# Kernel tuning notes

Hardware: AMD Instinct MI355X
Metric: run time of the kernel (lower is better)

## Reference

```python
import jax, jax.numpy as jnp
import numpy as np

T = 4096
HIDDEN = 2048
N_HEADS = 16
N_KV_HEADS = 4
HEAD_DIM = 128
WINDOW = 1024  # per_layer_sliding_window = WINDOW + 1 -> q attends keys with q_pos - k_pos <= WINDOW
ROPE_THETA = 100000.0
QKV_OUT = (N_HEADS + 2 * N_KV_HEADS) * HEAD_DIM  # 3072


def setup_inputs() -> dict:
    key = jax.random.key(0)
    k1, k2, k3, k4 = jax.random.split(key, 4)
    return {
        "hidden_states": jax.random.normal(k1, (T, HIDDEN), dtype=jnp.float32),
        "positions": jnp.arange(T, dtype=jnp.int32),
        "w_qkv": jax.random.normal(k2, (HIDDEN, QKV_OUT), dtype=jnp.float32) * 0.02,
        "b_qkv": jax.random.normal(k3, (QKV_OUT,), dtype=jnp.float32) * 0.02,
        "w_o": jax.random.normal(k4, (N_HEADS * HEAD_DIM, HIDDEN), dtype=jnp.float32) * 0.02,
    }


def _apply_rope(x, positions):
    # x: [T, n_heads, HEAD_DIM], neox-style rotary over full head dim
    half = HEAD_DIM // 2
    inv_freq = 1.0 / (ROPE_THETA ** (jnp.arange(half, dtype=jnp.float32) / half))
    freqs = positions.astype(jnp.float32)[:, None] * inv_freq[None, :]  # [T, half]
    cos = jnp.cos(freqs)[:, None, :]  # [T, 1, half]
    sin = jnp.sin(freqs)[:, None, :]
    x1, x2 = x[..., :half], x[..., half:]
    return jnp.concatenate([x1 * cos - x2 * sin, x2 * cos + x1 * sin], axis=-1)


def reference(hidden_states, positions, w_qkv, b_qkv, w_o):
    # QKV projection (bias=True)
    qkv = hidden_states @ w_qkv + b_qkv  # [T, QKV_OUT]
    q_size = N_HEADS * HEAD_DIM
    kv_size = N_KV_HEADS * HEAD_DIM
    q = qkv[:, :q_size].reshape(T, N_HEADS, HEAD_DIM)
    k = qkv[:, q_size:q_size + kv_size].reshape(T, N_KV_HEADS, HEAD_DIM)
    v = qkv[:, q_size + kv_size:].reshape(T, N_KV_HEADS, HEAD_DIM)

    # RoPE on q and k
    q = _apply_rope(q, positions)
    k = _apply_rope(k, positions)

    # GQA: expand kv heads to match query heads
    group = N_HEADS // N_KV_HEADS
    k = jnp.repeat(k, group, axis=1)  # [T, N_HEADS, HEAD_DIM]
    v = jnp.repeat(v, group, axis=1)

    scale = HEAD_DIM ** -0.5
    scores = jnp.einsum('qhd,khd->hqk', q, k) * scale  # [H, T, T]

    # causal + sliding-window mask: j <= i and i - j <= WINDOW
    i = jnp.arange(T)[:, None]
    j = jnp.arange(T)[None, :]
    mask = (j <= i) & (i - j <= WINDOW)  # [T, T]
    scores = jnp.where(mask[None, :, :], scores, jnp.finfo(scores.dtype).min)

    probs = jax.nn.softmax(scores, axis=-1)
    attn = jnp.einsum('hqk,khd->qhd', probs, v)  # [T, H, HEAD_DIM]
    attn = attn.reshape(T, N_HEADS * HEAD_DIM)

    # output projection (bias=False)
    return attn @ w_o
```

## Files before the change

### kernel.cpp

```cpp
#include <hip/hip_runtime.h>
#include <cstdint>

#define T_TOK 4096
#define HID 2048
#define NH 16
#define NKV 4
#define HD 128
#define WIN 1024
#define QKVO 3072

typedef float f32x4 __attribute__((ext_vector_type(4)));
typedef float f32x16 __attribute__((ext_vector_type(16)));
typedef __bf16 bf16x8 __attribute__((ext_vector_type(8)));
typedef __bf16 bf16x4 __attribute__((ext_vector_type(4)));
typedef unsigned int u32x4 __attribute__((ext_vector_type(4)));

__device__ __forceinline__ void gload16(const void* g, void* lds) {
  auto gp = reinterpret_cast<__attribute__((address_space(1))) void*>(
      reinterpret_cast<uintptr_t>(g));
  auto lp = reinterpret_cast<__attribute__((address_space(3))) void*>(
      reinterpret_cast<uintptr_t>(lds));
  __builtin_amdgcn_global_load_lds(gp, lp, 16, 0, 0);
}

__device__ __forceinline__ f32x4 mfma16(bf16x8 a, bf16x8 b, f32x4 c) {
  return __builtin_amdgcn_mfma_f32_16x16x32_bf16(a, b, c, 0, 0, 0);
}
__device__ __forceinline__ f32x16 mfma32(bf16x8 a, bf16x8 b, f32x16 c) {
  return __builtin_amdgcn_mfma_f32_32x32x16_bf16(a, b, c, 0, 0, 0);
}
__device__ __forceinline__ unsigned cvtpk(float lo, float hi) {
  unsigned r;
  asm("v_cvt_pk_bf16_f32 %0, %1, %2" : "=v"(r) : "v"(lo), "v"(hi));
  return r;
}
__device__ __forceinline__ void pl32swap(unsigned& a, unsigned& b) {
  asm volatile("v_permlane32_swap_b32 %0, %1" : "+v"(a), "+v"(b));
}

__global__ __launch_bounds__(256) void k_f32_to_bf16(const float* __restrict__ x,
                                                     __bf16* __restrict__ y) {
  const size_t e = (size_t)blockIdx.x * 256 + threadIdx.x;
  const float4* xv = (const float4*)x;
  float4 a = xv[e * 2], b = xv[e * 2 + 1];
  bf16x8 o;
  o[0] = (__bf16)a.x; o[1] = (__bf16)a.y; o[2] = (__bf16)a.z; o[3] = (__bf16)a.w;
  o[4] = (__bf16)b.x; o[5] = (__bf16)b.y; o[6] = (__bf16)b.z; o[7] = (__bf16)b.w;
  *(bf16x8*)(y + e * 8) = o;
}

__global__ __launch_bounds__(256) void k_transpose(const float* __restrict__ W,
                                                   __bf16* __restrict__ Wt,
                                                   int R, int C) {
  __shared__ __bf16 tb[32][33];
  const int nbx = C >> 5;
  const int c0 = (blockIdx.x % nbx) << 5;
  const int r0 = (blockIdx.x / nbx) << 5;
  const int tx = threadIdx.x & 31, ty = threadIdx.x >> 5;
#pragma unroll
  for (int i = 0; i < 32; i += 8)
    tb[ty + i][tx] = (__bf16)W[(size_t)(r0 + ty + i) * C + c0 + tx];
  __syncthreads();
#pragma unroll
  for (int i = 0; i < 32; i += 8)
    Wt[(size_t)(c0 + ty + i) * R + r0 + tx] = tb[tx][ty + i];
}

__global__ void k_rope_tab(const int* __restrict__ pos, float* __restrict__ cosT,
                           float* __restrict__ sinT) {
  const int t = blockIdx.x;
  const int d = threadIdx.x;
  const float inv = exp2f(-(float)d * (16.609640474436812f / 64.0f));
  const float fr = (float)pos[t] * inv;
  cosT[t * 64 + d] = cosf(fr);
  sinT[t * 64 + d] = sinf(fr);
}

template <bool BIAS, typename OutT>
__global__ __launch_bounds__(256, 2) void k_gemm(const __bf16* __restrict__ A,
                                                 const __bf16* __restrict__ Bt,
                                                 const float* __restrict__ bias,
                                                 OutT* __restrict__ C,
                                                 int M, int N, int K) {
  __shared__ __align__(16) __bf16 As[2][128 * 64];
  __shared__ __align__(16) __bf16 Bs[2][128 * 64];
  const int tid = threadIdx.x;
  const int lane = tid & 63;
  const int w = tid >> 6;
  const int wr = w >> 1, wc = w & 1;
  const int c = lane & 15, g = lane >> 4;
  const int csw = (c & 7) << 4;

  const int nstc = N >> 9;
  const int bid = blockIdx.x;
  const int xcd = bid & 7;
  const int j = bid >> 3;
  const int spx = (int)(gridDim.x >> 7);
  const int s = xcd * spx + (j >> 4);
  const int q = j & 15;
  const int by = (s / nstc) * 4 + (q >> 2);
  const int bx = (s % nstc) * 4 + (q & 3);
  const int m0 = by << 7, n0 = bx << 7;

  const int o0 = w * 4096 + lane * 16;
  const int srow = 32 * w + (lane >> 3);
  const int schunk = (lane & 7) ^ ((lane >> 3) & 7);
  const __bf16* gA0 = A + (size_t)(m0 + srow) * K + schunk * 8;
  const __bf16* gB0 = Bt + (size_t)(n0 + srow) * K + schunk * 8;

  f32x4 acc[4][4] = {};

  {
    char* la = (char*)&As[0][0];
    char* lb = (char*)&Bs[0][0];
#pragma unroll
    for (int qq = 0; qq < 4; qq++) {
      gload16(gA0 + (size_t)qq * 8 * K, la + o0 + qq * 1024);
      gload16(gB0 + (size_t)qq * 8 * K, lb + o0 + qq * 1024);
    }
  }
  __syncthreads();

  int cur = 0;
  for (int kt = 0; kt < K; kt += 64) {
    if (kt + 64 < K) {
      char* la = (char*)&As[0][0] + (cur ^ 1) * 16384;
      char* lb = (char*)&Bs[0][0] + (cur ^ 1) * 16384;
#pragma unroll
      for (int qq = 0; qq < 4; qq++) {
        gload16(gA0 + kt + 64 + (size_t)qq * 8 * K, la + o0 + qq * 1024);
        gload16(gB0 + kt + 64 + (size_t)qq * 8 * K, lb + o0 + qq * 1024);
      }
    }
    const char* as = (const char*)&As[0][0] + cur * 16384;
    const char* bs = (const char*)&Bs[0][0] + cur * 16384;
#pragma unroll
    for (int ds = 0; ds < 2; ds++) {
      bf16x8 af[4], bfr[4];
#pragma unroll
      for (int mi = 0; mi < 4; mi++)
        af[mi] = *(const bf16x8*)(as + (wr * 64 + mi * 16 + c) * 128 +
                                  ((ds * 64 + g * 16) ^ csw));
#pragma unroll
      for (int ni = 0; ni < 4; ni++)
        bfr[ni] = *(const bf16x8*)(bs + (wc * 64 + ni * 16 + c) * 128 +
                                   ((ds * 64 + g * 16) ^ csw));
#pragma unroll
      for (int mi = 0; mi < 4; mi++)
#pragma unroll
        for (int ni = 0; ni < 4; ni++)
          acc[mi][ni] = mfma16(af[mi], bfr[ni], acc[mi][ni]);
    }
    __syncthreads();
    cur ^= 1;
  }

#pragma unroll
  for (int ni = 0; ni < 4; ni++) {
    const int col = n0 + wc * 64 + ni * 16 + c;
    const float bv = BIAS ? bias[col] : 0.0f;
#pragma unroll
    for (int mi = 0; mi < 4; mi++)
#pragma unroll
      for (int r = 0; r < 4; r++) {
        const int row = m0 + wr * 64 + mi * 16 + 4 * g + r;
        C[(size_t)row * N + col] = (OutT)(acc[mi][ni][r] + bv);
      }
  }
}

__global__ __launch_bounds__(256) void k_rope_pack(
    const __bf16* __restrict__ qkv, const float* __restrict__ cosT,
    const float* __restrict__ sinT, __bf16* __restrict__ Qp,
    __bf16* __restrict__ Kp, __bf16* __restrict__ Vt) {
  const int t0 = blockIdx.x * 64;
  const int hh = blockIdx.y;
  const int tid = threadIdx.x;
  const int col0 = hh * HD;
  __shared__ __bf16 lt[64][136];
  if (hh < NH + NKV) {
    const bool isq = hh < NH;
    const float s = isq ? (0.08838834764831845f * 1.4426950408889634f) : 1.0f;
    __bf16* base = isq ? (Qp + (size_t)hh * T_TOK * HD)
                       : (Kp + (size_t)(hh - NH) * T_TOK * HD);
#pragma unroll
    for (int jj = 0; jj < 2; jj++) {
      const int e = jj * 256 + tid;
      const int tl = e >> 3, ch = e & 7;
      const int tt = t0 + tl;
      const bf16x8 x1 = *(const bf16x8*)(qkv + (size_t)tt * QKVO + col0 + ch * 8);
      const bf16x8 x2 = *(const bf16x8*)(qkv + (size_t)tt * QKVO + col0 + 64 + ch * 8);
      const float4 c0 = *(const float4*)(cosT + tt * 64 + ch * 8);
      const float4 c1 = *(const float4*)(cosT + tt * 64 + ch * 8 + 4);
      const float4 s0 = *(const float4*)(sinT + tt * 64 + ch * 8);
      const float4 s1 = *(const float4*)(sinT + tt * 64 + ch * 8 + 4);
      const float cs[8] = {c0.x, c0.y, c0.z, c0.w, c1.x, c1.y, c1.z, c1.w};
      const float sn[8] = {s0.x, s0.y, s0.z, s0.w, s1.x, s1.y, s1.z, s1.w};
      bf16x8 o1, o2;
#pragma unroll
      for (int i = 0; i < 8; i++) {
        const float a = (float)x1[i], b = (float)x2[i];
        o1[i] = (__bf16)((a * cs[i] - b * sn[i]) * s);
        o2[i] = (__bf16)((b * cs[i] + a * sn[i]) * s);
      }
      const int d2s = isq ? ch * 8 : ((ch * 8) ^ ((tt & 7) << 3));
      __bf16* dst = base + (size_t)tt * HD;
      *(bf16x8*)(dst + d2s) = o1;
      *(bf16x8*)(dst + 64 + d2s) = o2;
    }
  } else {
    const int kv = hh - (NH + NKV);
#pragma unroll
    for (int jj = 0; jj < 4; jj++) {
      const int e = jj * 256 + tid;
      const int tl = e >> 4, dc = e & 15;
      *(bf16x8*)&lt[tl][dc * 8] =
          *(const bf16x8*)(qkv + (size_t)(t0 + tl) * QKVO + col0 + dc * 8);
    }
    __syncthreads();
#pragma unroll
    for (int jj = 0; jj < 32; jj++) {
      const int e = jj * 256 + tid;
      const int d = e >> 6, tl = e & 63;
      Vt[((size_t)kv * HD + d) * T_TOK + t0 + (tl ^ ((d & 7) << 3))] = lt[tl][d];
    }
  }
}

__global__ __launch_bounds__(256, 2) void k_attn(const __bf16* __restrict__ Qp,
                                                 const __bf16* __restrict__ Kp,
                                                 const __bf16* __restrict__ Vt,
                                                 __bf16* __restrict__ attnO) {
  __shared__ __align__(16) __bf16 Ks[2][64 * 128];
  __shared__ __align__(16) __bf16 Vs[2][128 * 64];

  const int tid = threadIdx.x;
  const int lane = tid & 63;
  const int w = tid >> 6;
  const int l31 = lane & 31;
  const int hi = lane >> 5;
  const int swz = (lane & 7) << 4;
  const int h = blockIdx.y;
  const int kvh = h >> 2;
  const int qb = (int)(gridDim.x - 1) - (int)blockIdx.x;
  const int q0 = qb * 128;
  const int iw = q0 + 32 * w;
  const int irow = iw + l31;

  bf16x8 qf[8];
  {
    const __bf16* qbase = Qp + ((size_t)h * T_TOK + irow) * HD;
#pragma unroll
    for (int ds = 0; ds < 8; ds++)
      qf[ds] = *(const bf16x8*)(qbase + ds * 16 + hi * 8);
  }

  f32x16 ot[4] = {};
  float mrun = 0.0f, lrun = 0.0f;

  const int jstart = (q0 >= WIN) ? (q0 - WIN) : 0;
  const int niter = (q0 + 128 - jstart) >> 6;

  const char* Kg = (const char*)Kp + (size_t)kvh * T_TOK * HD * 2;
  const char* Vg = (const char*)Vt + (size_t)kvh * HD * T_TOK * 2;
  const char* kg0 = Kg + (size_t)(jstart + 16 * w + (lane >> 4)) * 256 + (lane & 15) * 16;
  const char* vg0 = Vg + (size_t)(32 * w + (lane >> 3)) * (T_TOK * 2) +
                    (size_t)jstart * 2 + (lane & 7) * 16;

#pragma unroll
  for (int q = 0; q < 4; q++)
    gload16(kg0 + q * 1024, (char*)&Ks[0][0] + w * 4096 + q * 1024);
#pragma unroll
  for (int q = 0; q < 4; q++)
    gload16(vg0 + (size_t)q * 8 * (T_TOK * 2), (char*)&Vs[0][0] + w * 4096 + q * 1024);

  int cur = 0;

  for (int it = 0; it < niter; ++it) {
    const int j0 = jstart + it * 64;
    __syncthreads();

    if (it + 1 < niter) {
      const char* kg = kg0 + (size_t)(it + 1) * 16384;
      const char* vg = vg0 + (size_t)(it + 1) * 128;
      char* kd = (char*)&Ks[cur ^ 1][0] + w * 4096;
      char* vd = (char*)&Vs[cur ^ 1][0] + w * 4096;
#pragma unroll
      for (int q = 0; q < 4; q++) gload16(kg + q * 1024, kd + q * 1024);
#pragma unroll
      for (int q = 0; q < 4; q++)
        gload16(vg + (size_t)q * 8 * (T_TOK * 2), vd + q * 1024);
    }

    if (j0 > iw + 31) { cur ^= 1; continue; }
    if (iw - (j0 + 63) > WIN) { cur ^= 1; continue; }

    const char* kb = (const char*)&Ks[cur][0];
    const char* vb = (const char*)&Vs[cur][0];

    f32x16 st[2] = {};
    __builtin_amdgcn_s_setprio(1);
#pragma unroll
    for (int t = 0; t < 2; t++)
#pragma unroll
      for (int ds = 0; ds < 8; ds++) {
        bf16x8 kf = *(const bf16x8*)(kb + (t * 32 + l31) * 256 +
                                     ((ds * 32 + hi * 16) ^ swz));
        st[t] = mfma32(kf, qf[ds], st[t]);
      }
    __builtin_amdgcn_s_setprio(0);

    float p[2][16];
    float cmax = -1e30f;
    const bool interior = (j0 + 63 <= iw) && (iw + 31 - j0 <= WIN);
    if (interior) {
#pragma unroll
      for (int t = 0; t < 2; t++)
#pragma unroll
        for (int r = 0; r < 16; r++) {
          const float s = st[t][r];
          p[t][r] = s;
          cmax = fmaxf(cmax, s);
        }
    } else {
      const int jb = irow - j0 - 4 * hi;
#pragma unroll
      for (int t = 0; t < 2; t++)
#pragma unroll
        for (int r = 0; r < 16; r++) {
          float s = st[t][r];
          const int off = 32 * t + (r & 3) + 8 * (r >> 2);
          s = ((unsigned)(jb - off) <= WIN) ? s : -1e30f;
          p[t][r] = s;
          cmax = fmaxf(cmax, s);
        }
    }
    cmax = fmaxf(cmax, __shfl_xor(cmax, 32));

    if (!__all(cmax <= mrun + 11.54f)) {
      const float mn = fmaxf(mrun, cmax);
      const float alpha = exp2f(mrun - mn);
      lrun *= alpha;
#pragma unroll
      for (int m = 0; m < 4; m++) ot[m] *= alpha;
      mrun = mn;
    }
    float rs = 0.0f;
#pragma unroll
    for (int t = 0; t < 2; t++)
#pragma unroll
      for (int r = 0; r < 16; r++) {
        const float e_ = exp2f(p[t][r] - mrun);
        p[t][r] = e_;
        rs += e_;
      }
    rs += __shfl_xor(rs, 32);
    lrun += rs;

    bf16x8 pb[4];
#pragma unroll
    for (int t = 0; t < 2; t++) {
      unsigned wds[8];
#pragma unroll
      for (int i = 0; i < 8; i++) wds[i] = cvtpk(p[t][2 * i], p[t][2 * i + 1]);
      pl32swap(wds[0], wds[2]);
      pl32swap(wds[1], wds[3]);
      pl32swap(wds[4], wds[6]);
      pl32swap(wds[5], wds[7]);
      u32x4 f0 = {wds[0], wds[1], wds[2], wds[3]};
      u32x4 f1 = {wds[4], wds[5], wds[6], wds[7]};
      pb[2 * t] = __builtin_bit_cast(bf16x8, f0);
      pb[2 * t + 1] = __builtin_bit_cast(bf16x8, f1);
    }

    __builtin_amdgcn_s_setprio(1);
#pragma unroll
    for (int m = 0; m < 4; m++) {
      const char* vrow = vb + (m * 32 + l31) * 128;
#pragma unroll
      for (int ks = 0; ks < 4; ks++) {
        bf16x8 vf = *(const bf16x8*)(vrow + ((ks * 32 + hi * 16) ^ swz));
        ot[m] = mfma32(vf, pb[ks], ot[m]);
      }
    }
    __builtin_amdgcn_s_setprio(0);

    cur ^= 1;
  }

  const float inv_l = 1.0f / lrun;
  __bf16* orow = attnO + (size_t)irow * (NH * HD) + h * HD;
#pragma unroll
  for (int m = 0; m < 4; m++)
#pragma unroll
    for (int rg = 0; rg < 4; rg++) {
      const int d0 = 32 * m + 8 * rg + 4 * hi;
      bf16x4 o4;
#pragma unroll
      for (int r = 0; r < 4; r++) o4[r] = (__bf16)(ot[m][4 * rg + r] * inv_l);
      *(bf16x4*)(orow + d0) = o4;
    }
}

extern "C" void kernel_launch(void* const* d_in, const int* in_sizes, int n_in,
                              void* d_out, int out_size, void* d_ws, size_t ws_size,
                              hipStream_t stream) {
  (void)in_sizes; (void)n_in; (void)out_size; (void)ws_size;
  const float* hidden = (const float*)d_in[0];
  const int* positions = (const int*)d_in[1];
  const float* w_qkv = (const float*)d_in[2];
  const float* b_qkv = (const float*)d_in[3];
  const float* w_o = (const float*)d_in[4];
  float* out = (float*)d_out;

  char* ws = (char*)d_ws;
  __bf16* Hb = (__bf16*)ws;    ws += (size_t)T_TOK * HID * 2;
  __bf16* Wqkvt = (__bf16*)ws; ws += (size_t)QKVO * HID * 2;
  __bf16* Wot = (__bf16*)ws;   ws += (size_t)HID * HID * 2;
  float* cosT = (float*)ws;    ws += (size_t)T_TOK * 64 * 4;
  float* sinT = (float*)ws;    ws += (size_t)T_TOK * 64 * 4;
  __bf16* qkv = (__bf16*)ws;   ws += (size_t)T_TOK * QKVO * 2;
  __bf16* Qp = (__bf16*)ws;    ws += (size_t)NH * T_TOK * HD * 2;
  __bf16* Kp = (__bf16*)ws;    ws += (size_t)NKV * T_TOK * HD * 2;
  __bf16* Vt = (__bf16*)ws;    ws += (size_t)NKV * HD * T_TOK * 2;
  __bf16* attnb = (__bf16*)ws; ws += (size_t)T_TOK * NH * HD * 2;

  k_f32_to_bf16<<<T_TOK * HID / (256 * 8), 256, 0, stream>>>(hidden, Hb);
  k_transpose<<<(QKVO / 32) * (HID / 32), 256, 0, stream>>>(w_qkv, Wqkvt, HID, QKVO);
  k_transpose<<<(HID / 32) * (HID / 32), 256, 0, stream>>>(w_o, Wot, HID, HID);
  k_rope_tab<<<T_TOK, 64, 0, stream>>>(positions, cosT, sinT);
  k_gemm<true, __bf16><<<(T_TOK / 128) * (QKVO / 128), 256, 0, stream>>>(
      Hb, Wqkvt, b_qkv, qkv, T_TOK, QKVO, HID);
  k_rope_pack<<<dim3(T_TOK / 64, NH + 2 * NKV), 256, 0, stream>>>(
      qkv, cosT, sinT, Qp, Kp, Vt);
  k_attn<<<dim3(T_TOK / 128, NH), 256, 0, stream>>>(Qp, Kp, Vt, attnb);
  k_gemm<false, float><<<(T_TOK / 128) * (HID / 128), 256, 0, stream>>>(
      attnb, Wot, nullptr, out, T_TOK, HID, HID);
}
```

Baseline: 185.0 us.

## Pre-pack V into MFMA fragment order and load directly to registers

The rope/pack kernel now writes V in a per-64-key tile layout that matches the MFMA operand fragment order per lane. The attention kernel drops the LDS double buffer for V and instead loads the V fragments straight from global memory into registers each iteration. This removes LDS traffic and LDS footprint for V, but puts uncached global load latency on the critical path without prefetching, and each wave reloads the same V tile, four waves times four heads sharing it.

```diff
diff --git a/kernel.cpp b/kernel.cpp
--- a/kernel.cpp
+++ b/kernel.cpp
@@ -172,7 +172,7 @@
 __global__ __launch_bounds__(256) void k_rope_pack(
     const __bf16* __restrict__ qkv, const float* __restrict__ cosT,
     const float* __restrict__ sinT, __bf16* __restrict__ Qp,
-    __bf16* __restrict__ Kp, __bf16* __restrict__ Vt) {
+    __bf16* __restrict__ Kp, __bf16* __restrict__ Vf) {
   const int t0 = blockIdx.x * 64;
   const int hh = blockIdx.y;
   const int tid = threadIdx.x;
@@ -218,21 +218,26 @@
           *(const bf16x8*)(qkv + (size_t)(t0 + tl) * QKVO + col0 + dc * 8);
     }
     __syncthreads();
-#pragma unroll
-    for (int jj = 0; jj < 32; jj++) {
-      const int e = jj * 256 + tid;
-      const int d = e >> 6, tl = e & 63;
-      Vt[((size_t)kv * HD + d) * T_TOK + t0 + (tl ^ ((d & 7) << 3))] = lt[tl][d];
+    __bf16* outb = Vf + ((size_t)kv * 64 + (t0 >> 6)) * 8192;
+#pragma unroll
+    for (int jj = 0; jj < 4; jj++) {
+      const int u = jj * 256 + tid;
+      const int lu = u & 63, ks = (u >> 6) & 3, m = u >> 8;
+      const int d = m * 32 + (lu & 31);
+      const int tb = ks * 16 + ((lu >> 5) << 3);
+      bf16x8 o;
+#pragma unroll
+      for (int j = 0; j < 8; j++) o[j] = lt[tb + j][d];
+      *(bf16x8*)(outb + (size_t)u * 8) = o;
     }
   }
 }
 
 __global__ __launch_bounds__(256, 2) void k_attn(const __bf16* __restrict__ Qp,
                                                  const __bf16* __restrict__ Kp,
-                                                 const __bf16* __restrict__ Vt,
+                                                 const __bf16* __restrict__ Vf,
                                                  __bf16* __restrict__ attnO) {
   __shared__ __align__(16) __bf16 Ks[2][64 * 128];
-  __shared__ __align__(16) __bf16 Vs[2][128 * 64];
 
   const int tid = threadIdx.x;
   const int lane = tid & 63;
@@ -262,17 +267,12 @@
   const int niter = (q0 + 128 - jstart) >> 6;
 
   const char* Kg = (const char*)Kp + (size_t)kvh * T_TOK * HD * 2;
-  const char* Vg = (const char*)Vt + (size_t)kvh * HD * T_TOK * 2;
   const char* kg0 = Kg + (size_t)(jstart + 16 * w + (lane >> 4)) * 256 + (lane & 15) * 16;
-  const char* vg0 = Vg + (size_t)(32 * w + (lane >> 3)) * (T_TOK * 2) +
-                    (size_t)jstart * 2 + (lane & 7) * 16;
+  const __bf16* Vgb = Vf + (size_t)kvh * 64 * 8192;
 
 #pragma unroll
   for (int q = 0; q < 4; q++)
     gload16(kg0 + q * 1024, (char*)&Ks[0][0] + w * 4096 + q * 1024);
-#pragma unroll
-  for (int q = 0; q < 4; q++)
-    gload16(vg0 + (size_t)q * 8 * (T_TOK * 2), (char*)&Vs[0][0] + w * 4096 + q * 1024);
 
   int cur = 0;
 
@@ -282,21 +282,23 @@
 
     if (it + 1 < niter) {
       const char* kg = kg0 + (size_t)(it + 1) * 16384;
-      const char* vg = vg0 + (size_t)(it + 1) * 128;
       char* kd = (char*)&Ks[cur ^ 1][0] + w * 4096;
-      char* vd = (char*)&Vs[cur ^ 1][0] + w * 4096;
 #pragma unroll
       for (int q = 0; q < 4; q++) gload16(kg + q * 1024, kd + q * 1024);
-#pragma unroll
-      for (int q = 0; q < 4; q++)
-        gload16(vg + (size_t)q * 8 * (T_TOK * 2), vd + q * 1024);
     }
 
     if (j0 > iw + 31) { cur ^= 1; continue; }
     if (iw - (j0 + 63) > WIN) { cur ^= 1; continue; }
 
+    const __bf16* vt = Vgb + (size_t)(j0 >> 6) * 8192;
+    bf16x8 vf[4][4];
+#pragma unroll
+    for (int m = 0; m < 4; m++)
+#pragma unroll
+      for (int ks = 0; ks < 4; ks++)
+        vf[m][ks] = *(const bf16x8*)(vt + (m * 256 + ks * 64 + lane) * 8);
+
     const char* kb = (const char*)&Ks[cur][0];
-    const char* vb = (const char*)&Vs[cur][0];
 
     f32x16 st[2] = {};
     __builtin_amdgcn_s_setprio(1);
@@ -375,14 +377,10 @@
 
     __builtin_amdgcn_s_setprio(1);
 #pragma unroll
-    for (int m = 0; m < 4; m++) {
-      const char* vrow = vb + (m * 32 + l31) * 128;
-#pragma unroll
-      for (int ks = 0; ks < 4; ks++) {
-        bf16x8 vf = *(const bf16x8*)(vrow + ((ks * 32 + hi * 16) ^ swz));
-        ot[m] = mfma32(vf, pb[ks], ot[m]);
-      }
-    }
+    for (int m = 0; m < 4; m++)
+#pragma unroll
+      for (int ks = 0; ks < 4; ks++)
+        ot[m] = mfma32(vf[m][ks], pb[ks], ot[m]);
     __builtin_amdgcn_s_setprio(0);
 
     cur ^= 1;
@@ -422,7 +420,7 @@
   __bf16* qkv = (__bf16*)ws;   ws += (size_t)T_TOK * QKVO * 2;
   __bf16* Qp = (__bf16*)ws;    ws += (size_t)NH * T_TOK * HD * 2;
   __bf16* Kp = (__bf16*)ws;    ws += (size_t)NKV * T_TOK * HD * 2;
-  __bf16* Vt = (__bf16*)ws;    ws += (size_t)NKV * HD * T_TOK * 2;
+  __bf16* Vfb = (__bf16*)ws;   ws += (size_t)NKV * 64 * 8192 * 2;
   __bf16* attnb = (__bf16*)ws; ws += (size_t)T_TOK * NH * HD * 2;
 
   k_f32_to_bf16<<<T_TOK * HID / (256 * 8), 256, 0, stream>>>(hidden, Hb);
@@ -432,8 +430,8 @@
   k_gemm<true, __bf16><<<(T_TOK / 128) * (QKVO / 128), 256, 0, stream>>>(
       Hb, Wqkvt, b_qkv, qkv, T_TOK, QKVO, HID);
   k_rope_pack<<<dim3(T_TOK / 64, NH + 2 * NKV), 256, 0, stream>>>(
-      qkv, cosT, sinT, Qp, Kp, Vt);
-  k_attn<<<dim3(T_TOK / 128, NH), 256, 0, stream>>>(Qp, Kp, Vt, attnb);
+      qkv, cosT, sinT, Qp, Kp, Vfb);
+  k_attn<<<dim3(T_TOK / 128, NH), 256, 0, stream>>>(Qp, Kp, Vfb, attnb);
   k_gemm<false, float><<<(T_TOK / 128) * (HID / 128), 256, 0, stream>>>(
       attnb, Wot, nullptr, out, T_TOK, HID, HID);
 }
```

After: 183.5 us. About the same (-0.8%).
